# Kernel optimization log

Hardware: AMD Instinct MI355X
Metric: run time of the kernel (lower is better)

Reference implementation:

```python
import jax, jax.numpy as jnp
import numpy as np

N_NODES = 200000
N_EDGES = 600000
NODE_IN = 32
EDGE_IN = 16
HID = 128
L = 3
MLP_HID = 128
LN_EPS = 1e-5


def _dense(k, fan_in, fan_out):
    kw, kb = jax.random.split(k)
    s = 1.0 / np.sqrt(fan_in)
    W = jax.random.uniform(kw, (fan_in, fan_out), jnp.float32, -s, s)
    b = jax.random.uniform(kb, (fan_out,), jnp.float32, -s, s)
    return W, b


def setup_inputs() -> dict:
    key = jax.random.key(0)
    ks = jax.random.split(key, 16)
    x = jax.random.normal(ks[0], (N_NODES, NODE_IN), jnp.float32)
    edge_index = jax.random.randint(ks[1], (2, N_EDGES), 0, N_NODES, jnp.int32)
    edge_attr = jax.random.normal(ks[2], (N_EDGES, EDGE_IN), jnp.float32)
    enc_w, enc_b = _dense(ks[3], NODE_IN, HID)
    ee_w, ee_b = _dense(ks[4], EDGE_IN, HID)
    w1s, b1s, w2s, b2s = [], [], [], []
    for i in range(L):
        W1, B1 = _dense(jax.random.fold_in(ks[5], i), HID, HID)
        W2, B2 = _dense(jax.random.fold_in(ks[6], i), HID, HID)
        w1s.append(W1); b1s.append(B1); w2s.append(W2); b2s.append(B2)
    gine_w1 = jnp.stack(w1s); gine_b1 = jnp.stack(b1s)
    gine_w2 = jnp.stack(w2s); gine_b2 = jnp.stack(b2s)
    gine_eps = jnp.zeros((L,), jnp.float32)  # PyG GINEConv default eps=0
    ln_g = jnp.ones((L, HID), jnp.float32)
    ln_b = jnp.zeros((L, HID), jnp.float32)
    mlp_w1, mlp_b1 = _dense(ks[7], 3 * HID, MLP_HID)
    mlp_w2, mlp_b2 = _dense(ks[8], MLP_HID, 1)
    return {"x": x, "edge_index": edge_index, "edge_attr": edge_attr,
            "enc_w": enc_w, "enc_b": enc_b, "ee_w": ee_w, "ee_b": ee_b,
            "gine_w1": gine_w1, "gine_b1": gine_b1, "gine_w2": gine_w2,
            "gine_b2": gine_b2, "gine_eps": gine_eps, "ln_g": ln_g, "ln_b": ln_b,
            "mlp_w1": mlp_w1, "mlp_b1": mlp_b1, "mlp_w2": mlp_w2, "mlp_b2": mlp_b2}


def reference(x, edge_index, edge_attr, enc_w, enc_b, ee_w, ee_b,
              gine_w1, gine_b1, gine_w2, gine_b2, gine_eps, ln_g, ln_b,
              mlp_w1, mlp_b1, mlp_w2, mlp_b2):
    src, dst = edge_index[0], edge_index[1]
    h = x @ enc_w + enc_b                      # [N, HID]
    e = edge_attr @ ee_w + ee_b                # [E, HID]
    for i in range(L):
        # GINEConv: out = MLP((1+eps)*x + sum_{j->i} relu(x_j + e_ji))
        msg = jax.nn.relu(h[src] + e)          # [E, HID] gather+fuse
        agg = jax.ops.segment_sum(msg, dst, num_segments=N_NODES)
        z = (1.0 + gine_eps[i]) * h + agg
        z = jax.nn.relu(z @ gine_w1[i] + gine_b1[i]) @ gine_w2[i] + gine_b2[i]
        # PyG LayerNorm (default mode='graph'): normalize over all nodes+features
        mu = jnp.mean(z)
        zc = z - mu
        var = jnp.mean(zc * zc)
        z = zc / jnp.sqrt(var + LN_EPS) * ln_g[i] + ln_b[i]
        h = jax.nn.relu(z)                     # dropout is identity at inference
    edge_inputs = jnp.concatenate([h[src], h[dst], e], axis=1)  # [E, 3*HID]
    hmid = jax.nn.relu(edge_inputs @ mlp_w1 + mlp_b1)
    logits = (hmid @ mlp_w2 + mlp_b2)[:, 0]    # [E]
    return logits
```

## Files before the change

### kernel.cpp

```cpp
#include <hip/hip_runtime.h>
#include <hip/hip_bf16.h>

#define N_NODES 200000
#define N_EDGES 600000
#define NODE_IN 32
#define EDGE_IN 16
#define HID     128
#define LN_EPS  1e-5f

typedef __attribute__((ext_vector_type(8))) short short8;
typedef __attribute__((ext_vector_type(4))) float f32x4;

static __device__ __forceinline__ ushort f2b(float f) {
    unsigned u = __builtin_bit_cast(unsigned, f);
    unsigned r = (u + 0x7fffu + ((u >> 16) & 1u)) >> 16;
    return (ushort)r;
}
static __device__ __forceinline__ float b2f(ushort us) {
    unsigned u = ((unsigned)us) << 16;
    return __builtin_bit_cast(float, u);
}

__global__ __launch_bounds__(256) void k_prep_g(
    const float* __restrict__ gw1, const float* __restrict__ gw2,
    ushort* __restrict__ wpk)
{
    const int gidx = blockIdx.x * 256 + threadIdx.x;
    const int m    = gidx >> 11;
    const int r    = gidx & 2047;
    const int lane = r & 63;
    const int ntkb = r >> 6;
    const int nt = ntkb & 7, kb = ntkb >> 3;
    const int n  = nt * 16 + (lane & 15);
    const int k0 = kb * 32 + (lane >> 4) * 8;
    const float* W = (m < 3) ? gw1 + (size_t)m * HID * HID
                             : gw2 + (size_t)(m - 3) * HID * HID;
    short8 v;
#pragma unroll
    for (int j = 0; j < 8; j++)
        v[j] = (short)f2b(W[(size_t)(k0 + j) * HID + n]);
    ((short8*)wpk)[gidx] = v;
}

__global__ __launch_bounds__(256) void k_prep_m(
    const float* __restrict__ mw1, ushort* __restrict__ w1p)
{
    const int gidx = blockIdx.x * 256 + threadIdx.x;
    const int lane = gidx & 63;
    const int ntkb = gidx >> 6;
    const int nt = ntkb & 7, kb = ntkb >> 3;
    const int n  = nt * 16 + (lane & 15);
    const int k0 = kb * 32 + (lane >> 4) * 8;
    short8 v;
#pragma unroll
    for (int j = 0; j < 8; j++)
        v[j] = (short)f2b(mw1[(size_t)(k0 + j) * HID + n]);
    ((short8*)w1p)[gidx] = v;
}

__global__ __launch_bounds__(256) void k_node_enc(
    const float* __restrict__ x, const float* __restrict__ w,
    const float* __restrict__ b, const float* __restrict__ epsp,
    ushort* __restrict__ hb, float* __restrict__ agg,
    float* __restrict__ red)
{
    __shared__ float sx[16][NODE_IN];
    const int tid = threadIdx.x;
    const int n0  = blockIdx.x * 16;
    float* sxf = &sx[0][0];
    sxf[tid]       = x[(size_t)n0 * NODE_IN + tid];
    sxf[tid + 256] = x[(size_t)n0 * NODE_IN + tid + 256];

    const int f   = tid & 127;
    const int grp = tid >> 7;
    float wcol[NODE_IN];
#pragma unroll
    for (int k = 0; k < NODE_IN; k++) wcol[k] = w[k * HID + f];
    const float bf = b[f];
    const float alpha = 1.0f + epsp[0];
    __syncthreads();

#pragma unroll
    for (int it = 0; it < 8; it++) {
        const int ln = it * 2 + grp;
        const int n  = n0 + ln;
        const float4* sx4 = (const float4*)sx[ln];
        float acc = bf;
#pragma unroll
        for (int k4 = 0; k4 < NODE_IN / 4; k4++) {
            float4 v = sx4[k4];
            acc += v.x * wcol[k4*4] + v.y * wcol[k4*4+1] +
                   v.z * wcol[k4*4+2] + v.w * wcol[k4*4+3];
        }
        hb[(size_t)n * HID + f]  = f2b(acc);
        agg[(size_t)n * HID + f] = alpha * acc;
    }
    if (blockIdx.x == 0 && tid == 0) { red[0] = 0.f; red[1] = 0.f; }
}

__global__ __launch_bounds__(256) void k_msg(
    const ushort* __restrict__ hb, const int* __restrict__ ei,
    const float* __restrict__ ea, const float* __restrict__ eew,
    const float* __restrict__ eeb, float* __restrict__ agg)
{
    __shared__ float sea[16][EDGE_IN];
    const int* __restrict__ src = ei;
    const int* __restrict__ dst = ei + N_EDGES;
    const int tid = threadIdx.x;
    const int e0  = blockIdx.x * 16;
    ((float*)sea)[tid] = ea[(size_t)e0 * EDGE_IN + tid];

    const int f   = tid & 127;
    const int grp = tid >> 7;
    float wcol[EDGE_IN];
#pragma unroll
    for (int k = 0; k < EDGE_IN; k++) wcol[k] = eew[k * HID + f];
    const float bf = eeb[f];
    __syncthreads();

#pragma unroll
    for (int it = 0; it < 8; it++) {
        const int le = it * 2 + grp;
        const int e  = e0 + le;
        const int s  = src[e];
        const int d  = dst[e];
        const float4* se4 = (const float4*)sea[le];
        float ev = bf;
#pragma unroll
        for (int k4 = 0; k4 < EDGE_IN / 4; k4++) {
            float4 v = se4[k4];
            ev += v.x * wcol[k4*4] + v.y * wcol[k4*4+1] +
                  v.z * wcol[k4*4+2] + v.w * wcol[k4*4+3];
        }
        float m = b2f(hb[(size_t)s * HID + f]) + ev;
        m = fmaxf(m, 0.f);
        atomicAdd(&agg[(size_t)d * HID + f], m);
    }
}

template<bool IN_BF16, bool RELU_OUT, bool REDUCE>
__global__ __launch_bounds__(256) void k_gemm(
    const void* in_, const short8* __restrict__ wp,
    const float* __restrict__ bias, ushort* out, float* __restrict__ red)
{
    __shared__ ushort sU[64][136];
    const int tid = threadIdx.x;
    const int m0  = blockIdx.x * 64;

    if constexpr (IN_BF16) {
        const short8* in8 = (const short8*)((const ushort*)in_ + (size_t)m0 * HID);
#pragma unroll
        for (int it = 0; it < 4; it++) {
            const int q = it * 256 + tid;
            const int r = q >> 4, c8 = q & 15;
            *(short8*)&sU[r][c8 * 8] = in8[q];
        }
    } else {
        const float4* in4 = (const float4*)((const float*)in_ + (size_t)m0 * HID);
#pragma unroll
        for (int it = 0; it < 8; it++) {
            const int q = it * 256 + tid;
            const int r = q >> 5, c4 = q & 31;
            float4 v = in4[q];
            ushort4 u;
            u.x = f2b(v.x); u.y = f2b(v.y); u.z = f2b(v.z); u.w = f2b(v.w);
            *(ushort4*)&sU[r][c4 * 4] = u;
        }
    }
    __syncthreads();

    const int lane = tid & 63;
    const int r0   = (tid >> 6) * 16;
    const int arow = r0 + (lane & 15);
    const int kg8  = (lane >> 4) * 8;
    f32x4 acc[8] = {};
    for (int kb = 0; kb < 4; kb++) {
        short8 af = *(const short8*)&sU[arow][kb * 32 + kg8];
#pragma unroll
        for (int nt = 0; nt < 8; nt++) {
            short8 bf8 = wp[(kb * 8 + nt) * 64 + lane];
            acc[nt] = __builtin_amdgcn_mfma_f32_16x16x32_bf16(af, bf8, acc[nt], 0, 0, 0);
        }
    }

    float lsum = 0.f, lsq = 0.f;
    const int rowb = m0 + r0 + (lane >> 4) * 4;
#pragma unroll
    for (int nt = 0; nt < 8; nt++) {
        const int c = nt * 16 + (lane & 15);
        const float bc = bias[c];
#pragma unroll
        for (int j = 0; j < 4; j++) {
            float o = acc[nt][j] + bc;
            if constexpr (RELU_OUT) o = fmaxf(o, 0.f);
            if constexpr (REDUCE) { lsum += o; lsq += o * o; }
            out[(size_t)(rowb + j) * HID + c] = f2b(o);
        }
    }

    if constexpr (REDUCE) {
#pragma unroll
        for (int off = 32; off; off >>= 1) {
            lsum += __shfl_down(lsum, off);
            lsq  += __shfl_down(lsq, off);
        }
        __shared__ float sws[4], swq[4];
        const int wid = tid >> 6;
        if ((tid & 63) == 0) { sws[wid] = lsum; swq[wid] = lsq; }
        __syncthreads();
        if (tid == 0) {
            atomicAdd(&red[0], sws[0] + sws[1] + sws[2] + sws[3]);
            atomicAdd(&red[1], swq[0] + swq[1] + swq[2] + swq[3]);
        }
    }
}

__global__ void k_lnfin(float* __restrict__ red)
{
    if (threadIdx.x == 0) {
        const float inv = 1.0f / ((float)N_NODES * (float)HID);
        const float mu  = red[0] * inv;
        const float var = red[1] * inv - mu * mu;
        red[2] = mu;
        red[3] = 1.0f / sqrtf(var + LN_EPS);
        red[0] = 0.f; red[1] = 0.f;
    }
}

template<bool FUSE_NEXT>
__global__ __launch_bounds__(256) void k_ln(
    const ushort* __restrict__ zb, const float* __restrict__ red,
    const float* __restrict__ g, const float* __restrict__ b,
    ushort* __restrict__ hb, const float* __restrict__ eps_next,
    float* __restrict__ agg)
{
    const float mu = red[2], rstd = red[3];
    const int i = blockIdx.x * 256 + threadIdx.x;
    short8 z8 = ((const short8*)zb)[i];
    const int cb = (i & 15) * 2;
    float4 g0 = ((const float4*)g)[cb],  g1 = ((const float4*)g)[cb + 1];
    float4 b0 = ((const float4*)b)[cb],  b1 = ((const float4*)b)[cb + 1];
    float o[8];
    o[0] = fmaxf((b2f((ushort)z8[0]) - mu) * rstd * g0.x + b0.x, 0.f);
    o[1] = fmaxf((b2f((ushort)z8[1]) - mu) * rstd * g0.y + b0.y, 0.f);
    o[2] = fmaxf((b2f((ushort)z8[2]) - mu) * rstd * g0.z + b0.z, 0.f);
    o[3] = fmaxf((b2f((ushort)z8[3]) - mu) * rstd * g0.w + b0.w, 0.f);
    o[4] = fmaxf((b2f((ushort)z8[4]) - mu) * rstd * g1.x + b1.x, 0.f);
    o[5] = fmaxf((b2f((ushort)z8[5]) - mu) * rstd * g1.y + b1.y, 0.f);
    o[6] = fmaxf((b2f((ushort)z8[6]) - mu) * rstd * g1.z + b1.z, 0.f);
    o[7] = fmaxf((b2f((ushort)z8[7]) - mu) * rstd * g1.w + b1.w, 0.f);
    short8 h8;
#pragma unroll
    for (int j = 0; j < 8; j++) h8[j] = (short)f2b(o[j]);
    ((short8*)hb)[i] = h8;
    if constexpr (FUSE_NEXT) {
        const float a = 1.0f + eps_next[0];
        float4 A0, A1;
        A0.x = a*o[0]; A0.y = a*o[1]; A0.z = a*o[2]; A0.w = a*o[3];
        A1.x = a*o[4]; A1.y = a*o[5]; A1.z = a*o[6]; A1.w = a*o[7];
        ((float4*)agg)[i * 2]     = A0;
        ((float4*)agg)[i * 2 + 1] = A1;
    }
}

__global__ __launch_bounds__(256) void k_mlp(
    const ushort* __restrict__ hb, const int* __restrict__ ei,
    const float* __restrict__ ea, const float* __restrict__ eew,
    const float* __restrict__ eeb,
    const ushort* __restrict__ w1p, const float* __restrict__ b1,
    const float* __restrict__ w2, const float* __restrict__ b2,
    float* __restrict__ out)
{
    __shared__ ushort sU[64][392];
    const int* __restrict__ src = ei;
    const int* __restrict__ dst = ei + N_EDGES;
    const int tid = threadIdx.x;
    const int e0  = blockIdx.x * 64;

    const short8* hb8 = (const short8*)hb;
#pragma unroll
    for (int it = 0; it < 8; it++) {
        const int q = it * 256 + tid;
        const int e = q >> 5;
        const int c = q & 31;
        const int node = (c < 16) ? src[e0 + e] : dst[e0 + e];
        short8 v = hb8[(size_t)node * 16 + (c & 15)];
        *(short8*)&sU[e][c * 8] = v;
    }

    {
        const int f = tid & 127;
        float wcol[EDGE_IN];
#pragma unroll
        for (int k = 0; k < EDGE_IN; k++) wcol[k] = eew[k * HID + f];
        const float bf = eeb[f];
#pragma unroll
        for (int it = 0; it < 32; it++) {
            const int e = it * 2 + (tid >> 7);
            const float4* ea4 = (const float4*)(ea + (size_t)(e0 + e) * EDGE_IN);
            float ev = bf;
#pragma unroll
            for (int k4 = 0; k4 < EDGE_IN / 4; k4++) {
                float4 v = ea4[k4];
                ev += v.x * wcol[k4*4] + v.y * wcol[k4*4+1] +
                      v.z * wcol[k4*4+2] + v.w * wcol[k4*4+3];
            }
            sU[e][256 + f] = f2b(ev);
        }
    }
    __syncthreads();

    const int lane = tid & 63;
    const int wv   = tid >> 6;
    const int r0   = wv * 16;
    const int arow = r0 + (lane & 15);
    const int kgrp = lane >> 4;
    f32x4 acc[8] = {};
    const short8* bfr = (const short8*)w1p;
    for (int kb = 0; kb < 12; kb++) {
        short8 afrag = *(const short8*)&sU[arow][kb * 32 + kgrp * 8];
#pragma unroll
        for (int nt = 0; nt < 8; nt++) {
            short8 bfrag = bfr[(kb * 8 + nt) * 64 + lane];
            acc[nt] = __builtin_amdgcn_mfma_f32_16x16x32_bf16(afrag, bfrag, acc[nt], 0, 0, 0);
        }
    }

    float s0 = 0.f, s1 = 0.f, s2 = 0.f, s3 = 0.f;
#pragma unroll
    for (int nt = 0; nt < 8; nt++) {
        const int col = nt * 16 + (lane & 15);
        const float b1c = b1[col];
        const float w2c = w2[col];
        s0 += fmaxf(acc[nt][0] + b1c, 0.f) * w2c;
        s1 += fmaxf(acc[nt][1] + b1c, 0.f) * w2c;
        s2 += fmaxf(acc[nt][2] + b1c, 0.f) * w2c;
        s3 += fmaxf(acc[nt][3] + b1c, 0.f) * w2c;
    }
#pragma unroll
    for (int m = 1; m < 16; m <<= 1) {
        s0 += __shfl_xor(s0, m); s1 += __shfl_xor(s1, m);
        s2 += __shfl_xor(s2, m); s3 += __shfl_xor(s3, m);
    }
    if ((lane & 15) == 0) {
        const float bb = b2[0];
        const int eb = e0 + r0 + kgrp * 4;
        out[eb + 0] = s0 + bb; out[eb + 1] = s1 + bb;
        out[eb + 2] = s2 + bb; out[eb + 3] = s3 + bb;
    }
}

extern "C" void kernel_launch(void* const* d_in, const int* in_sizes, int n_in,
                              void* d_out, int out_size, void* d_ws, size_t ws_size,
                              hipStream_t stream)
{
    const float* x    = (const float*)d_in[0];
    const int*   ei   = (const int*)  d_in[1];
    const float* ea   = (const float*)d_in[2];
    const float* encw = (const float*)d_in[3];
    const float* encb = (const float*)d_in[4];
    const float* eew  = (const float*)d_in[5];
    const float* eeb  = (const float*)d_in[6];
    const float* gw1  = (const float*)d_in[7];
    const float* gb1  = (const float*)d_in[8];
    const float* gw2  = (const float*)d_in[9];
    const float* gb2  = (const float*)d_in[10];
    const float* geps = (const float*)d_in[11];
    const float* lng  = (const float*)d_in[12];
    const float* lnb  = (const float*)d_in[13];
    const float* mw1  = (const float*)d_in[14];
    const float* mb1  = (const float*)d_in[15];
    const float* mw2  = (const float*)d_in[16];
    const float* mb2  = (const float*)d_in[17];

    float* ws = (float*)d_ws;
    const size_t NH = (size_t)N_NODES * HID;
    float*  agg = ws;
    ushort* zb  = (ushort*)(ws + NH);
    ushort* hb  = (ushort*)(ws + NH + NH / 2);
    float*  red = ws + 2 * NH;

    ushort* wpk = (ushort*)d_out;

    k_prep_g<<<48, 256, 0, stream>>>(gw1, gw2, wpk);
    k_node_enc<<<N_NODES / 16, 256, 0, stream>>>(x, encw, encb, geps, hb, agg, red);

    const int LN_BLKS = (int)(NH / 8 / 256);
    for (int l = 0; l < 3; l++) {
        k_msg<<<N_EDGES / 16, 256, 0, stream>>>(hb, ei, ea, eew, eeb, agg);
        k_gemm<false, true, false><<<N_NODES / 64, 256, 0, stream>>>(
            agg, (const short8*)wpk + (size_t)l * 2048,
            gb1 + (size_t)l * HID, zb, nullptr);
        k_gemm<true, false, true><<<N_NODES / 64, 256, 0, stream>>>(
            zb, (const short8*)wpk + (size_t)(3 + l) * 2048,
            gb2 + (size_t)l * HID, zb, red);
        k_lnfin<<<1, 64, 0, stream>>>(red);
        if (l < 2)
            k_ln<true><<<LN_BLKS, 256, 0, stream>>>(
                zb, red, lng + (size_t)l * HID, lnb + (size_t)l * HID, hb,
                geps + l + 1, agg);
        else
            k_ln<false><<<LN_BLKS, 256, 0, stream>>>(
                zb, red, lng + (size_t)l * HID, lnb + (size_t)l * HID, hb,
                nullptr, nullptr);
    }

    ushort* w1p = (ushort*)agg;
    k_prep_m<<<24, 256, 0, stream>>>(mw1, w1p);
    k_mlp<<<N_EDGES / 64, 256, 0, stream>>>(hb, ei, ea, eew, eeb,
                                            w1p, mb1, mw2, mb2, (float*)d_out);
}
```

Baseline: 1.602 ms.

## Build dst-sorted CSR once and aggregate per node instead of atomics

Builds a CSR index of incoming edges per destination node (degree count, scan, fill) once per call. Message aggregation then runs one block half per node, summing over its in-edges in registers and doing a single read-modify-write, which removes the float atomicAdds on agg. The final edge MLP now loads node feature fragments straight into MFMA operands from global memory instead of staging them in LDS, and h and z share one buffer. The cost is seven extra small kernels for CSR setup, load imbalance from varying degree, and uncoalesced edge-id indirection.

```diff
diff --git a/kernel.cpp b/kernel.cpp
--- a/kernel.cpp
+++ b/kernel.cpp
@@ -7,6 +7,8 @@
 #define EDGE_IN 16
 #define HID     128
 #define LN_EPS  1e-5f
+#define SCAN_B  512
+#define NBLK_SCAN 391
 
 typedef __attribute__((ext_vector_type(8))) short short8;
 typedef __attribute__((ext_vector_type(4))) float f32x4;
@@ -19,6 +21,74 @@
 static __device__ __forceinline__ float b2f(ushort us) {
     unsigned u = ((unsigned)us) << 16;
     return __builtin_bit_cast(float, u);
+}
+
+__global__ __launch_bounds__(256) void k_csr_zero(int* __restrict__ deg)
+{
+    const int i = blockIdx.x * 256 + threadIdx.x;
+    if (i < N_NODES) deg[i] = 0;
+}
+
+__global__ __launch_bounds__(256) void k_csr_deg(
+    const int* __restrict__ ei, int* __restrict__ deg)
+{
+    const int e = blockIdx.x * 256 + threadIdx.x;
+    if (e < N_EDGES) atomicAdd(&deg[ei[N_EDGES + e]], 1);
+}
+
+__global__ __launch_bounds__(SCAN_B) void k_scan1(
+    const int* __restrict__ deg, int* __restrict__ part)
+{
+    __shared__ int s[SCAN_B];
+    const int t = threadIdx.x, i = blockIdx.x * SCAN_B + t;
+    s[t] = (i < N_NODES) ? deg[i] : 0;
+    __syncthreads();
+    for (int off = SCAN_B / 2; off; off >>= 1) {
+        if (t < off) s[t] += s[t + off];
+        __syncthreads();
+    }
+    if (t == 0) part[blockIdx.x] = s[0];
+}
+
+__global__ void k_scan2(int* __restrict__ part, int* __restrict__ rowptr)
+{
+    if (threadIdx.x == 0) {
+        int run = 0;
+        for (int b = 0; b < NBLK_SCAN; b++) { int x = part[b]; part[b] = run; run += x; }
+        rowptr[N_NODES] = N_EDGES;
+    }
+}
+
+__global__ __launch_bounds__(SCAN_B) void k_scan3(
+    const int* __restrict__ deg, const int* __restrict__ part,
+    int* __restrict__ rowptr, int* __restrict__ cursor)
+{
+    __shared__ int s[SCAN_B];
+    const int t = threadIdx.x, i = blockIdx.x * SCAN_B + t;
+    const int v = (i < N_NODES) ? deg[i] : 0;
+    s[t] = v;
+    __syncthreads();
+    for (int off = 1; off < SCAN_B; off <<= 1) {
+        int x = (t >= off) ? s[t - off] : 0;
+        __syncthreads();
+        s[t] += x;
+        __syncthreads();
+    }
+    if (i < N_NODES) {
+        const int ex = s[t] - v + part[blockIdx.x];
+        rowptr[i] = ex;
+        cursor[i] = ex;
+    }
+}
+
+__global__ __launch_bounds__(256) void k_csr_fill(
+    const int* __restrict__ ei, int* __restrict__ cursor, int* __restrict__ eid)
+{
+    const int e = blockIdx.x * 256 + threadIdx.x;
+    if (e < N_EDGES) {
+        const int slot = atomicAdd(&cursor[ei[N_EDGES + e]], 1);
+        eid[slot] = e;
+    }
 }
 
 __global__ __launch_bounds__(256) void k_prep_g(
@@ -98,44 +168,38 @@
     if (blockIdx.x == 0 && tid == 0) { red[0] = 0.f; red[1] = 0.f; }
 }
 
-__global__ __launch_bounds__(256) void k_msg(
+__global__ __launch_bounds__(256) void k_agg(
     const ushort* __restrict__ hb, const int* __restrict__ ei,
     const float* __restrict__ ea, const float* __restrict__ eew,
-    const float* __restrict__ eeb, float* __restrict__ agg)
-{
-    __shared__ float sea[16][EDGE_IN];
+    const float* __restrict__ eeb,
+    const int* __restrict__ rowptr, const int* __restrict__ eid,
+    float* __restrict__ agg)
+{
+    const int tid = threadIdx.x;
+    const int n   = blockIdx.x * 2 + (tid >> 7);
+    const int f   = tid & 127;
     const int* __restrict__ src = ei;
-    const int* __restrict__ dst = ei + N_EDGES;
-    const int tid = threadIdx.x;
-    const int e0  = blockIdx.x * 16;
-    ((float*)sea)[tid] = ea[(size_t)e0 * EDGE_IN + tid];
-
-    const int f   = tid & 127;
-    const int grp = tid >> 7;
+
     float wcol[EDGE_IN];
 #pragma unroll
     for (int k = 0; k < EDGE_IN; k++) wcol[k] = eew[k * HID + f];
     const float bf = eeb[f];
-    __syncthreads();
-
-#pragma unroll
-    for (int it = 0; it < 8; it++) {
-        const int le = it * 2 + grp;
-        const int e  = e0 + le;
-        const int s  = src[e];
-        const int d  = dst[e];
-        const float4* se4 = (const float4*)sea[le];
+
+    float s = 0.f;
+    const int beg = rowptr[n], end = rowptr[n + 1];
+    for (int j = beg; j < end; j++) {
+        const int e  = eid[j];
+        const int sn = src[e];
+        const float4* ea4 = (const float4*)(ea + (size_t)e * EDGE_IN);
+        float4 a0 = ea4[0], a1 = ea4[1], a2 = ea4[2], a3 = ea4[3];
         float ev = bf;
-#pragma unroll
-        for (int k4 = 0; k4 < EDGE_IN / 4; k4++) {
-            float4 v = se4[k4];
-            ev += v.x * wcol[k4*4] + v.y * wcol[k4*4+1] +
-                  v.z * wcol[k4*4+2] + v.w * wcol[k4*4+3];
-        }
-        float m = b2f(hb[(size_t)s * HID + f]) + ev;
-        m = fmaxf(m, 0.f);
-        atomicAdd(&agg[(size_t)d * HID + f], m);
-    }
+        ev += a0.x*wcol[0]  + a0.y*wcol[1]  + a0.z*wcol[2]  + a0.w*wcol[3];
+        ev += a1.x*wcol[4]  + a1.y*wcol[5]  + a1.z*wcol[6]  + a1.w*wcol[7];
+        ev += a2.x*wcol[8]  + a2.y*wcol[9]  + a2.z*wcol[10] + a2.w*wcol[11];
+        ev += a3.x*wcol[12] + a3.y*wcol[13] + a3.z*wcol[14] + a3.w*wcol[15];
+        s += fmaxf(b2f(hb[(size_t)sn * HID + f]) + ev, 0.f);
+    }
+    agg[(size_t)n * HID + f] += s;
 }
 
 template<bool IN_BF16, bool RELU_OUT, bool REDUCE>
@@ -229,14 +293,13 @@
 
 template<bool FUSE_NEXT>
 __global__ __launch_bounds__(256) void k_ln(
-    const ushort* __restrict__ zb, const float* __restrict__ red,
+    ushort* zh, const float* __restrict__ red,
     const float* __restrict__ g, const float* __restrict__ b,
-    ushort* __restrict__ hb, const float* __restrict__ eps_next,
-    float* __restrict__ agg)
+    const float* __restrict__ eps_next, float* __restrict__ agg)
 {
     const float mu = red[2], rstd = red[3];
     const int i = blockIdx.x * 256 + threadIdx.x;
-    short8 z8 = ((const short8*)zb)[i];
+    short8 z8 = ((const short8*)zh)[i];
     const int cb = (i & 15) * 2;
     float4 g0 = ((const float4*)g)[cb],  g1 = ((const float4*)g)[cb + 1];
     float4 b0 = ((const float4*)b)[cb],  b1 = ((const float4*)b)[cb + 1];
@@ -252,7 +315,7 @@
     short8 h8;
 #pragma unroll
     for (int j = 0; j < 8; j++) h8[j] = (short)f2b(o[j]);
-    ((short8*)hb)[i] = h8;
+    ((short8*)zh)[i] = h8;
     if constexpr (FUSE_NEXT) {
         const float a = 1.0f + eps_next[0];
         float4 A0, A1;
@@ -271,22 +334,14 @@
     const float* __restrict__ w2, const float* __restrict__ b2,
     float* __restrict__ out)
 {
-    __shared__ ushort sU[64][392];
+    __shared__ ushort sE[64][136];
     const int* __restrict__ src = ei;
     const int* __restrict__ dst = ei + N_EDGES;
     const int tid = threadIdx.x;
     const int e0  = blockIdx.x * 64;
-
-    const short8* hb8 = (const short8*)hb;
-#pragma unroll
-    for (int it = 0; it < 8; it++) {
-        const int q = it * 256 + tid;
-        const int e = q >> 5;
-        const int c = q & 31;
-        const int node = (c < 16) ? src[e0 + e] : dst[e0 + e];
-        short8 v = hb8[(size_t)node * 16 + (c & 15)];
-        *(short8*)&sU[e][c * 8] = v;
-    }
+    const int lane = tid & 63;
+    const int wv   = tid >> 6;
+    const int r0   = wv * 16;
 
     {
         const int f = tid & 127;
@@ -305,24 +360,38 @@
                 ev += v.x * wcol[k4*4] + v.y * wcol[k4*4+1] +
                       v.z * wcol[k4*4+2] + v.w * wcol[k4*4+3];
             }
-            sU[e][256 + f] = f2b(ev);
-        }
-    }
+            sE[e][f] = f2b(ev);
+        }
+    }
+
+    const int er = e0 + r0 + (lane & 15);
+    const int kg = lane >> 4;
+    const int ns = src[er], nd = dst[er];
+    const short8* hb8 = (const short8*)hb;
+    short8 af[8];
+#pragma unroll
+    for (int kb = 0; kb < 4; kb++) af[kb]     = hb8[(size_t)ns * 16 + kb * 4 + kg];
+#pragma unroll
+    for (int kb = 0; kb < 4; kb++) af[4 + kb] = hb8[(size_t)nd * 16 + kb * 4 + kg];
     __syncthreads();
 
-    const int lane = tid & 63;
-    const int wv   = tid >> 6;
-    const int r0   = wv * 16;
-    const int arow = r0 + (lane & 15);
-    const int kgrp = lane >> 4;
     f32x4 acc[8] = {};
     const short8* bfr = (const short8*)w1p;
-    for (int kb = 0; kb < 12; kb++) {
-        short8 afrag = *(const short8*)&sU[arow][kb * 32 + kgrp * 8];
+#pragma unroll
+    for (int kb = 0; kb < 8; kb++) {
 #pragma unroll
         for (int nt = 0; nt < 8; nt++) {
             short8 bfrag = bfr[(kb * 8 + nt) * 64 + lane];
-            acc[nt] = __builtin_amdgcn_mfma_f32_16x16x32_bf16(afrag, bfrag, acc[nt], 0, 0, 0);
+            acc[nt] = __builtin_amdgcn_mfma_f32_16x16x32_bf16(af[kb], bfrag, acc[nt], 0, 0, 0);
+        }
+    }
+#pragma unroll
+    for (int kb = 8; kb < 12; kb++) {
+        short8 ae = *(const short8*)&sE[r0 + (lane & 15)][(kb - 8) * 32 + kg * 8];
+#pragma unroll
+        for (int nt = 0; nt < 8; nt++) {
+            short8 bfrag = bfr[(kb * 8 + nt) * 64 + lane];
+            acc[nt] = __builtin_amdgcn_mfma_f32_16x16x32_bf16(ae, bfrag, acc[nt], 0, 0, 0);
         }
     }
 
@@ -344,7 +413,7 @@
     }
     if ((lane & 15) == 0) {
         const float bb = b2[0];
-        const int eb = e0 + r0 + kgrp * 4;
+        const int eb = e0 + r0 + kg * 4;
         out[eb + 0] = s0 + bb; out[eb + 1] = s1 + bb;
         out[eb + 2] = s2 + bb; out[eb + 3] = s3 + bb;
     }
@@ -376,37 +445,50 @@
     float* ws = (float*)d_ws;
     const size_t NH = (size_t)N_NODES * HID;
     float*  agg = ws;
-    ushort* zb  = (ushort*)(ws + NH);
-    ushort* hb  = (ushort*)(ws + NH + NH / 2);
+    ushort* zh  = (ushort*)(ws + NH);
+    int*    csr = (int*)(ws + NH + NH / 2);
     float*  red = ws + 2 * NH;
 
+    int* deg    = csr;
+    int* rowptr = csr + 200000;
+    int* cursor = csr + 400064;
+    int* eid    = csr + 600064;
+    int* part   = csr + 1200064;
+
     ushort* wpk = (ushort*)d_out;
 
     k_prep_g<<<48, 256, 0, stream>>>(gw1, gw2, wpk);
-    k_node_enc<<<N_NODES / 16, 256, 0, stream>>>(x, encw, encb, geps, hb, agg, red);
+    k_csr_zero<<<(N_NODES + 255) / 256, 256, 0, stream>>>(deg);
+    k_csr_deg<<<(N_EDGES + 255) / 256, 256, 0, stream>>>(ei, deg);
+    k_scan1<<<NBLK_SCAN, SCAN_B, 0, stream>>>(deg, part);
+    k_scan2<<<1, 64, 0, stream>>>(part, rowptr);
+    k_scan3<<<NBLK_SCAN, SCAN_B, 0, stream>>>(deg, part, rowptr, cursor);
+    k_csr_fill<<<(N_EDGES + 255) / 256, 256, 0, stream>>>(ei, cursor, eid);
+    k_node_enc<<<N_NODES / 16, 256, 0, stream>>>(x, encw, encb, geps, zh, agg, red);
 
     const int LN_BLKS = (int)(NH / 8 / 256);
     for (int l = 0; l < 3; l++) {
-        k_msg<<<N_EDGES / 16, 256, 0, stream>>>(hb, ei, ea, eew, eeb, agg);
+        k_agg<<<N_NODES / 2, 256, 0, stream>>>(zh, ei, ea, eew, eeb,
+                                               rowptr, eid, agg);
         k_gemm<false, true, false><<<N_NODES / 64, 256, 0, stream>>>(
             agg, (const short8*)wpk + (size_t)l * 2048,
-            gb1 + (size_t)l * HID, zb, nullptr);
+            gb1 + (size_t)l * HID, zh, nullptr);
         k_gemm<true, false, true><<<N_NODES / 64, 256, 0, stream>>>(
-            zb, (const short8*)wpk + (size_t)(3 + l) * 2048,
-            gb2 + (size_t)l * HID, zb, red);
+            zh, (const short8*)wpk + (size_t)(3 + l) * 2048,
+            gb2 + (size_t)l * HID, zh, red);
         k_lnfin<<<1, 64, 0, stream>>>(red);
         if (l < 2)
             k_ln<true><<<LN_BLKS, 256, 0, stream>>>(
-                zb, red, lng + (size_t)l * HID, lnb + (size_t)l * HID, hb,
+                zh, red, lng + (size_t)l * HID, lnb + (size_t)l * HID,
                 geps + l + 1, agg);
         else
             k_ln<false><<<LN_BLKS, 256, 0, stream>>>(
-                zb, red, lng + (size_t)l * HID, lnb + (size_t)l * HID, hb,
+                zh, red, lng + (size_t)l * HID, lnb + (size_t)l * HID,
                 nullptr, nullptr);
     }
 
     ushort* w1p = (ushort*)agg;
     k_prep_m<<<24, 256, 0, stream>>>(mw1, w1p);
-    k_mlp<<<N_EDGES / 64, 256, 0, stream>>>(hb, ei, ea, eew, eeb,
+    k_mlp<<<N_EDGES / 64, 256, 0, stream>>>(zh, ei, ea, eew, eeb,
                                             w1p, mb1, mw2, mb2, (float*)d_out);
 }
```

Result: slower. 1.793 ms (+12.0%).
